# Kernel tuning notes

Measured on AMD Instinct MI355X. Metric: run time of the kernel, lower is better.

## Reference

```python
import jax, jax.numpy as jnp
import numpy as np

EPS = 1e-8

def setup_inputs() -> dict:
    key = jax.random.key(0)
    k1, k2, k3, k4, k5 = jax.random.split(key, 5)
    B, S, d, H = 4, 1024, 512, 8
    hd = d // H
    x = jax.random.normal(k1, (B, S, d), dtype=jnp.float32)
    V = jax.random.normal(k2, (B, S, H, hd), dtype=jnp.float32)
    # binary biological mask [B, S, S]
    M = (jax.random.uniform(k3, (B, S, S)) > 0.5).astype(jnp.float32)
    in_proj_w = jax.random.normal(k4, (3 * d, d), dtype=jnp.float32) * 0.02
    in_proj_b = jnp.zeros((3 * d,), dtype=jnp.float32)
    out_w = jax.random.normal(k5, (d, d), dtype=jnp.float32) * 0.02
    out_b = jnp.zeros((d,), dtype=jnp.float32)
    return {"x": x, "V": V, "M": M, "in_proj_w": in_proj_w,
            "in_proj_b": in_proj_b, "out_w": out_w, "out_b": out_b}


def reference(x, V, M, in_proj_w, in_proj_b, out_w, out_b):
    B, S, d = x.shape
    H, hd = V.shape[2], V.shape[3]
    # packed QKV projection (torch MHA in_proj); V slice is computed by torch
    # but its result is discarded, so only Q,K slices influence the output.
    qkv = x @ in_proj_w.T + in_proj_b            # [B, S, 3d]
    q = qkv[..., :d].reshape(B, S, H, hd).transpose(0, 2, 1, 3)        # [B,H,S,hd]
    k = qkv[..., d:2 * d].reshape(B, S, H, hd).transpose(0, 2, 1, 3)   # [B,H,S,hd]
    scores = jnp.einsum("bhqd,bhkd->bhqk", q, k) / jnp.sqrt(jnp.float32(hd))
    A = jax.nn.softmax(scores, axis=-1)           # [B,H,S,S] per-head attn weights
    # biological mask + L1 renormalization (post-hoc, as in original)
    A_sparse = A * M[:, None, :, :]
    norm = jnp.sum(jnp.abs(A_sparse), axis=-1, keepdims=True) + EPS
    A_bar = A_sparse / norm
    # custom V: [B,S,H,hd] -> [B,H,S,hd]
    Vp = V.transpose(0, 2, 1, 3)
    out = jnp.einsum("bhqk,bhkd->bhqd", A_bar, Vp)  # [B,H,S,hd]
    out = out.transpose(0, 2, 1, 3).reshape(B, S, d)
    return out @ out_w.T + out_b
```

## Files before the change

kernel.cpp:

```cpp
#include <hip/hip_runtime.h>
#include <hip/hip_bf16.h>

#define BB 4
#define SS 1024
#define DD 512
#define HH 8
#define HD 64

typedef __attribute__((ext_vector_type(8))) short bf16x8;
typedef __attribute__((ext_vector_type(4))) float f32x4;

static __device__ __forceinline__ unsigned short f2b(float f) {
  union { float f; unsigned int u; } c; c.f = f;
  return (unsigned short)((c.u + 0x7fffu + ((c.u >> 16) & 1u)) >> 16);
}

__global__ __launch_bounds__(256) void prep(
    const float* __restrict__ x, const float* __restrict__ W1,
    const float* __restrict__ Wo, const float* __restrict__ Mmask,
    const float* __restrict__ V, unsigned short* __restrict__ xb,
    unsigned short* __restrict__ W1b, unsigned short* __restrict__ Wob,
    unsigned char* __restrict__ Mpack, unsigned short* __restrict__ Vt) {
  __shared__ float Ls[64][65];
  const int bid = blockIdx.x;
  const int tid = threadIdx.x;

  if (bid < 1408) {
    const float* src; unsigned short* dst; size_t off;
    if (bid < 1024) { src = x;  dst = xb;  off = ((size_t)bid * 256 + tid) * 8; }
    else if (bid < 1280) { src = W1; dst = W1b; off = ((size_t)(bid - 1024) * 256 + tid) * 8; }
    else { src = Wo; dst = Wob; off = ((size_t)(bid - 1280) * 256 + tid) * 8; }
    const float4 a = *(const float4*)(src + off);
    const float4 b = *(const float4*)(src + off + 4);
    union { unsigned short s[8]; uint4 v; } o;
    o.s[0] = f2b(a.x); o.s[1] = f2b(a.y); o.s[2] = f2b(a.z); o.s[3] = f2b(a.w);
    o.s[4] = f2b(b.x); o.s[5] = f2b(b.y); o.s[6] = f2b(b.z); o.s[7] = f2b(b.w);
    *(uint4*)(dst + off) = o.v;
  } else if (bid < 3456) {
    const size_t g = (size_t)(bid - 1408) * 256 + tid;
    const float4 a = *(const float4*)(Mmask + g * 8);
    const float4 b = *(const float4*)(Mmask + g * 8 + 4);
    unsigned v = 0;
    v |= (a.x > 0.5f) ? 1u : 0u;   v |= (a.y > 0.5f) ? 2u : 0u;
    v |= (a.z > 0.5f) ? 4u : 0u;   v |= (a.w > 0.5f) ? 8u : 0u;
    v |= (b.x > 0.5f) ? 16u : 0u;  v |= (b.y > 0.5f) ? 32u : 0u;
    v |= (b.z > 0.5f) ? 64u : 0u;  v |= (b.w > 0.5f) ? 128u : 0u;
    Mpack[g] = (unsigned char)v;
  } else {
    const int id = bid - 3456;
    const int s0 = (id & 15) * 64, h = (id >> 4) & 7, b = id >> 7;
    {
      const int r = tid >> 2, cs = (tid & 3) * 16;
      const float* src = V + ((size_t)((b * SS + s0 + r) * HH) + h) * HD + cs;
#pragma unroll
      for (int j = 0; j < 4; j++) {
        const float4 v = *(const float4*)(src + j * 4);
        Ls[r][cs + j * 4 + 0] = v.x; Ls[r][cs + j * 4 + 1] = v.y;
        Ls[r][cs + j * 4 + 2] = v.z; Ls[r][cs + j * 4 + 3] = v.w;
      }
    }
    __syncthreads();
    {
      const int d = tid >> 2, ss = (tid & 3) * 16;
      union { unsigned short s[16]; uint4 v[2]; } o;
#pragma unroll
      for (int j = 0; j < 16; j++) o.s[j] = f2b(Ls[ss + j][d]);
      unsigned short* dst =
          Vt + ((size_t)((b * HH + h) * HD + d)) * SS + s0 + ss;
      *(uint4*)dst = o.v[0];
      *(uint4*)(dst + 8) = o.v[1];
    }
  }
}

__global__ __launch_bounds__(256) void gemm_qk(
    const unsigned short* __restrict__ xb, const unsigned short* __restrict__ W1b,
    const float* __restrict__ bias, unsigned short* __restrict__ qkb) {
  __shared__ unsigned short As[128][72];
  __shared__ unsigned short Bs[64][72];
  const int tid = threadIdx.x;
  const int lane = tid & 63, wave = tid >> 6;
  const int l16 = lane & 15, quad = lane >> 4;
  const int row0 = blockIdx.y * 128, col0 = blockIdx.x * 64;

  f32x4 acc[2][4];
#pragma unroll
  for (int i = 0; i < 2; i++)
#pragma unroll
    for (int j = 0; j < 4; j++) acc[i][j] = (f32x4){0.f, 0.f, 0.f, 0.f};

  for (int k0 = 0; k0 < DD; k0 += 64) {
    __syncthreads();
    {
      const int r = tid >> 1, cs = (tid & 1) * 32;
      const unsigned short* s = xb + (size_t)(row0 + r) * DD + k0 + cs;
#pragma unroll
      for (int j = 0; j < 4; j++)
        *(uint4*)&As[r][cs + j * 8] = *(const uint4*)(s + j * 8);
    }
    {
      const int r = tid >> 2, cs = (tid & 3) * 16;
      const unsigned short* s = W1b + (size_t)(col0 + r) * DD + k0 + cs;
      *(uint4*)&Bs[r][cs] = *(const uint4*)s;
      *(uint4*)&Bs[r][cs + 8] = *(const uint4*)(s + 8);
    }
    __syncthreads();

#pragma unroll
    for (int kk = 0; kk < 64; kk += 32) {
      const bf16x8 a0 = *(const bf16x8*)&As[wave * 32 + l16][kk + quad * 8];
      const bf16x8 a1 = *(const bf16x8*)&As[wave * 32 + 16 + l16][kk + quad * 8];
#pragma unroll
      for (int nt = 0; nt < 4; nt++) {
        const bf16x8 bb = *(const bf16x8*)&Bs[nt * 16 + l16][kk + quad * 8];
        acc[0][nt] = __builtin_amdgcn_mfma_f32_16x16x32_bf16(a0, bb, acc[0][nt], 0, 0, 0);
        acc[1][nt] = __builtin_amdgcn_mfma_f32_16x16x32_bf16(a1, bb, acc[1][nt], 0, 0, 0);
      }
    }
  }

#pragma unroll
  for (int nt = 0; nt < 4; nt++) {
    const int col = col0 + nt * 16 + l16;
    const float bv = bias[col];
    const float scale = (col < DD) ? 0.125f : 1.0f;
#pragma unroll
    for (int mi = 0; mi < 2; mi++)
#pragma unroll
      for (int reg = 0; reg < 4; reg++) {
        const int row = row0 + wave * 32 + mi * 16 + quad * 4 + reg;
        qkb[(size_t)row * 1024 + col] = f2b((acc[mi][nt][reg] + bv) * scale);
      }
  }
}

__global__ __launch_bounds__(256) void gemm_out(
    const unsigned short* __restrict__ Ab, const unsigned short* __restrict__ Wob,
    const float* __restrict__ bias, float* __restrict__ out) {
  __shared__ unsigned short As[128][72];
  __shared__ unsigned short Bs[64][72];
  const int tid = threadIdx.x;
  const int lane = tid & 63, wave = tid >> 6;
  const int l16 = lane & 15, quad = lane >> 4;
  const int row0 = blockIdx.y * 128, col0 = blockIdx.x * 64;

  f32x4 acc[2][4];
#pragma unroll
  for (int i = 0; i < 2; i++)
#pragma unroll
    for (int j = 0; j < 4; j++) acc[i][j] = (f32x4){0.f, 0.f, 0.f, 0.f};

  for (int k0 = 0; k0 < DD; k0 += 64) {
    __syncthreads();
    {
      const int r = tid >> 1, cs = (tid & 1) * 32;
      const unsigned short* s = Ab + (size_t)(row0 + r) * DD + k0 + cs;
#pragma unroll
      for (int j = 0; j < 4; j++)
        *(uint4*)&As[r][cs + j * 8] = *(const uint4*)(s + j * 8);
    }
    {
      const int r = tid >> 2, cs = (tid & 3) * 16;
      const unsigned short* s = Wob + (size_t)(col0 + r) * DD + k0 + cs;
      *(uint4*)&Bs[r][cs] = *(const uint4*)s;
      *(uint4*)&Bs[r][cs + 8] = *(const uint4*)(s + 8);
    }
    __syncthreads();

#pragma unroll
    for (int kk = 0; kk < 64; kk += 32) {
      const bf16x8 a0 = *(const bf16x8*)&As[wave * 32 + l16][kk + quad * 8];
      const bf16x8 a1 = *(const bf16x8*)&As[wave * 32 + 16 + l16][kk + quad * 8];
#pragma unroll
      for (int nt = 0; nt < 4; nt++) {
        const bf16x8 bb = *(const bf16x8*)&Bs[nt * 16 + l16][kk + quad * 8];
        acc[0][nt] = __builtin_amdgcn_mfma_f32_16x16x32_bf16(a0, bb, acc[0][nt], 0, 0, 0);
        acc[1][nt] = __builtin_amdgcn_mfma_f32_16x16x32_bf16(a1, bb, acc[1][nt], 0, 0, 0);
      }
    }
  }

#pragma unroll
  for (int nt = 0; nt < 4; nt++) {
    const int col = col0 + nt * 16 + l16;
    const float bv = bias[col];
#pragma unroll
    for (int mi = 0; mi < 2; mi++)
#pragma unroll
      for (int reg = 0; reg < 4; reg++) {
        const int row = row0 + wave * 32 + mi * 16 + quad * 4 + reg;
        out[(size_t)row * DD + col] = acc[mi][nt][reg] + bv;
      }
  }
}

__global__ __launch_bounds__(256) void flash_attn(
    const unsigned short* __restrict__ qkb, const unsigned short* __restrict__ Vt,
    const unsigned char* __restrict__ Mpack, unsigned short* __restrict__ attnb) {
  __shared__ unsigned short Qs[64][72];
  __shared__ unsigned short Ks[64][72];
  __shared__ unsigned short Vs[64][72];
  __shared__ unsigned short Ps[4][16][72];
  __shared__ float SmT[4][16];

  const int tid = threadIdx.x;
  const int lane = tid & 63, wave = tid >> 6;
  const int l16 = lane & 15, quad = lane >> 4;
  const int q0 = blockIdx.x * 64;
  const int h = blockIdx.y;
  const int b = blockIdx.z;

  {
    const int r = tid >> 2, cs = (tid & 3) * 16;
    const unsigned short* s = qkb + (size_t)(b * SS + q0 + r) * 1024 + h * HD + cs;
    *(uint4*)&Qs[r][cs] = *(const uint4*)s;
    *(uint4*)&Qs[r][cs + 8] = *(const uint4*)(s + 8);
  }
  const bf16x8 bQ0 = *(const bf16x8*)&Qs[wave * 16 + l16][quad * 8];
  const bf16x8 bQ1 = *(const bf16x8*)&Qs[wave * 16 + l16][32 + quad * 8];

  const unsigned char* mrowp =
      Mpack + (size_t)(b * SS + q0 + wave * 16 + l16) * 128;

  float Smp = 0.f;
  f32x4 O[4];
#pragma unroll
  for (int i = 0; i < 4; i++) O[i] = (f32x4){0.f, 0.f, 0.f, 0.f};

  const unsigned short* kbase = qkb + (size_t)(b * SS) * 1024 + DD + h * HD;
  const unsigned short* vbase = Vt + (size_t)((b * HH + h) * HD) * SS;

#pragma unroll 2
  for (int i = 0; i < 16; i++) {
    const uint2 mm = *(const uint2*)(mrowp + i * 8);

    __syncthreads();
    {
      const int r = tid >> 2, cs = (tid & 3) * 16;
      const unsigned short* s = kbase + (size_t)(i * 64 + r) * 1024 + cs;
      *(uint4*)&Ks[r][cs] = *(const uint4*)s;
      *(uint4*)&Ks[r][cs + 8] = *(const uint4*)(s + 8);
      const unsigned short* v = vbase + (size_t)r * SS + i * 64 + cs;
      *(uint4*)&Vs[r][cs] = *(const uint4*)v;
      *(uint4*)&Vs[r][cs + 8] = *(const uint4*)(v + 8);
    }
    __syncthreads();

#pragma unroll
    for (int t = 0; t < 4; t++) {
      const bf16x8 aK0 = *(const bf16x8*)&Ks[t * 16 + l16][quad * 8];
      const bf16x8 aK1 = *(const bf16x8*)&Ks[t * 16 + l16][32 + quad * 8];
      f32x4 a = (f32x4){0.f, 0.f, 0.f, 0.f};
      a = __builtin_amdgcn_mfma_f32_16x16x32_bf16(aK0, bQ0, a, 0, 0, 0);
      a = __builtin_amdgcn_mfma_f32_16x16x32_bf16(aK1, bQ1, a, 0, 0, 0);
      const unsigned nib =
          ((t < 2 ? mm.x : mm.y) >> ((t & 1) * 16 + quad * 4)) & 0xFu;
      float e0 = __expf(a[0]); e0 = (nib & 1u) ? e0 : 0.f;
      float e1 = __expf(a[1]); e1 = (nib & 2u) ? e1 : 0.f;
      float e2 = __expf(a[2]); e2 = (nib & 4u) ? e2 : 0.f;
      float e3 = __expf(a[3]); e3 = (nib & 8u) ? e3 : 0.f;
      Smp += (e0 + e1) + (e2 + e3);
      uint2 w;
      w.x = (unsigned)f2b(e0) | ((unsigned)f2b(e1) << 16);
      w.y = (unsigned)f2b(e2) | ((unsigned)f2b(e3) << 16);
      *(uint2*)&Ps[wave][l16][t * 16 + quad * 4] = w;
    }

    const bf16x8 aP0 = *(const bf16x8*)&Ps[wave][l16][quad * 8];
    const bf16x8 aP1 = *(const bf16x8*)&Ps[wave][l16][32 + quad * 8];
#pragma unroll
    for (int dt = 0; dt < 4; dt++) {
      const bf16x8 bV0 = *(const bf16x8*)&Vs[dt * 16 + l16][quad * 8];
      const bf16x8 bV1 = *(const bf16x8*)&Vs[dt * 16 + l16][32 + quad * 8];
      O[dt] = __builtin_amdgcn_mfma_f32_16x16x32_bf16(aP0, bV0, O[dt], 0, 0, 0);
      O[dt] = __builtin_amdgcn_mfma_f32_16x16x32_bf16(aP1, bV1, O[dt], 0, 0, 0);
    }
  }

  Smp += __shfl_xor(Smp, 16);
  Smp += __shfl_xor(Smp, 32);
  if (lane < 16) SmT[wave][lane] = Smp;
  float invr[4];
#pragma unroll
  for (int reg = 0; reg < 4; reg++)
    invr[reg] = 1.0f / (SmT[wave][quad * 4 + reg] + 1e-12f);
#pragma unroll
  for (int reg = 0; reg < 4; reg++) {
    const size_t row = (size_t)(b * SS + q0 + wave * 16 + quad * 4 + reg);
#pragma unroll
    for (int dt = 0; dt < 4; dt++)
      attnb[row * DD + h * HD + dt * 16 + l16] = f2b(O[dt][reg] * invr[reg]);
  }
}

extern "C" void kernel_launch(void* const* d_in, const int* in_sizes, int n_in,
                              void* d_out, int out_size, void* d_ws,
                              size_t ws_size, hipStream_t stream) {
  const float* x = (const float*)d_in[0];
  const float* V = (const float*)d_in[1];
  const float* Mmask = (const float*)d_in[2];
  const float* in_proj_w = (const float*)d_in[3];
  const float* in_proj_b = (const float*)d_in[4];
  const float* out_w = (const float*)d_in[5];
  const float* out_b = (const float*)d_in[6];
  float* out = (float*)d_out;

  unsigned char* ws = (unsigned char*)d_ws;
  unsigned short* qkb   = (unsigned short*)(ws);
  unsigned short* xb    = (unsigned short*)(ws + (8ull << 20));
  unsigned short* W1b   = (unsigned short*)(ws + (12ull << 20));
  unsigned short* Wob   = (unsigned short*)(ws + (13ull << 20));
  unsigned short* Vt    = (unsigned short*)(ws + (14ull << 20));
  unsigned short* attnb = (unsigned short*)(ws + (18ull << 20));
  unsigned char*  Mpack = ws + (22ull << 20);

  prep<<<3968, 256, 0, stream>>>(x, in_proj_w, out_w, Mmask, V,
                                 xb, W1b, Wob, Mpack, Vt);
  gemm_qk<<<dim3(16, 32), 256, 0, stream>>>(xb, W1b, in_proj_b, qkb);
  flash_attn<<<dim3(SS / 64, HH, BB), 256, 0, stream>>>(qkb, Vt, Mpack, attnb);
  gemm_out<<<dim3(8, 32), 256, 0, stream>>>(attnb, Wob, out_b, out);
}
```

Baseline: 149.6 us.

## Fuse all stages into one persistent kernel with grid-wide barriers

Merges the prep, QK projection, masked attention and output projection kernels into a single persistent kernel of 512 blocks. The stages are separated by atomic-counter grid barriers, and a union overlays their shared-memory buffers. The aim is to remove three kernel launch gaps and the tail drain between stages. The output GEMM is retiled to 64x64 so that it also fits exactly 512 blocks. In exchange, all blocks must be co-resident for the spin barriers to be safe, there is a memset launch per call, and the 64x64 tiles give less reuse in the final GEMM.

```diff
diff --git a/kernel.cpp b/kernel.cpp
--- a/kernel.cpp
+++ b/kernel.cpp
@@ -6,6 +6,7 @@
 #define DD 512
 #define HH 8
 #define HD 64
+#define NBLK 512u
 
 typedef __attribute__((ext_vector_type(8))) short bf16x8;
 typedef __attribute__((ext_vector_type(4))) float f32x4;
@@ -15,281 +16,275 @@
   return (unsigned short)((c.u + 0x7fffu + ((c.u >> 16) & 1u)) >> 16);
 }
 
-__global__ __launch_bounds__(256) void prep(
-    const float* __restrict__ x, const float* __restrict__ W1,
-    const float* __restrict__ Wo, const float* __restrict__ Mmask,
-    const float* __restrict__ V, unsigned short* __restrict__ xb,
-    unsigned short* __restrict__ W1b, unsigned short* __restrict__ Wob,
-    unsigned char* __restrict__ Mpack, unsigned short* __restrict__ Vt) {
-  __shared__ float Ls[64][65];
-  const int bid = blockIdx.x;
-  const int tid = threadIdx.x;
-
-  if (bid < 1408) {
-    const float* src; unsigned short* dst; size_t off;
-    if (bid < 1024) { src = x;  dst = xb;  off = ((size_t)bid * 256 + tid) * 8; }
-    else if (bid < 1280) { src = W1; dst = W1b; off = ((size_t)(bid - 1024) * 256 + tid) * 8; }
-    else { src = Wo; dst = Wob; off = ((size_t)(bid - 1280) * 256 + tid) * 8; }
-    const float4 a = *(const float4*)(src + off);
-    const float4 b = *(const float4*)(src + off + 4);
-    union { unsigned short s[8]; uint4 v; } o;
-    o.s[0] = f2b(a.x); o.s[1] = f2b(a.y); o.s[2] = f2b(a.z); o.s[3] = f2b(a.w);
-    o.s[4] = f2b(b.x); o.s[5] = f2b(b.y); o.s[6] = f2b(b.z); o.s[7] = f2b(b.w);
-    *(uint4*)(dst + off) = o.v;
-  } else if (bid < 3456) {
-    const size_t g = (size_t)(bid - 1408) * 256 + tid;
-    const float4 a = *(const float4*)(Mmask + g * 8);
-    const float4 b = *(const float4*)(Mmask + g * 8 + 4);
-    unsigned v = 0;
-    v |= (a.x > 0.5f) ? 1u : 0u;   v |= (a.y > 0.5f) ? 2u : 0u;
-    v |= (a.z > 0.5f) ? 4u : 0u;   v |= (a.w > 0.5f) ? 8u : 0u;
-    v |= (b.x > 0.5f) ? 16u : 0u;  v |= (b.y > 0.5f) ? 32u : 0u;
-    v |= (b.z > 0.5f) ? 64u : 0u;  v |= (b.w > 0.5f) ? 128u : 0u;
-    Mpack[g] = (unsigned char)v;
-  } else {
-    const int id = bid - 3456;
-    const int s0 = (id & 15) * 64, h = (id >> 4) & 7, b = id >> 7;
-    {
-      const int r = tid >> 2, cs = (tid & 3) * 16;
-      const float* src = V + ((size_t)((b * SS + s0 + r) * HH) + h) * HD + cs;
-#pragma unroll
-      for (int j = 0; j < 4; j++) {
-        const float4 v = *(const float4*)(src + j * 4);
-        Ls[r][cs + j * 4 + 0] = v.x; Ls[r][cs + j * 4 + 1] = v.y;
-        Ls[r][cs + j * 4 + 2] = v.z; Ls[r][cs + j * 4 + 3] = v.w;
-      }
-    }
-    __syncthreads();
-    {
-      const int d = tid >> 2, ss = (tid & 3) * 16;
-      union { unsigned short s[16]; uint4 v[2]; } o;
-#pragma unroll
-      for (int j = 0; j < 16; j++) o.s[j] = f2b(Ls[ss + j][d]);
-      unsigned short* dst =
-          Vt + ((size_t)((b * HH + h) * HD + d)) * SS + s0 + ss;
-      *(uint4*)dst = o.v[0];
-      *(uint4*)(dst + 8) = o.v[1];
-    }
-  }
+static __device__ __forceinline__ void grid_barrier(unsigned* cnt) {
+  __threadfence();
+  __syncthreads();
+  if (threadIdx.x == 0) {
+    __hip_atomic_fetch_add(cnt, 1u, __ATOMIC_ACQ_REL, __HIP_MEMORY_SCOPE_AGENT);
+    while (__hip_atomic_load(cnt, __ATOMIC_ACQUIRE, __HIP_MEMORY_SCOPE_AGENT) <
+           NBLK)
+      __builtin_amdgcn_s_sleep(2);
+  }
+  __syncthreads();
+  __threadfence();
 }
 
-__global__ __launch_bounds__(256) void gemm_qk(
-    const unsigned short* __restrict__ xb, const unsigned short* __restrict__ W1b,
-    const float* __restrict__ bias, unsigned short* __restrict__ qkb) {
-  __shared__ unsigned short As[128][72];
-  __shared__ unsigned short Bs[64][72];
+union SharedU {
+  struct { float Ls[64][65]; } pr;
+  struct { unsigned short As[128][72], Bs[64][72]; } gm;
+  struct {
+    unsigned short Qs[64][72], Ks[64][72], Vs[64][72], Ps[4][16][72];
+    float SmT[4][16];
+  } fl;
+};
+
+__global__ __launch_bounds__(256, 2) void fused(
+    const float* __restrict__ x, const float* __restrict__ V,
+    const float* __restrict__ Mmask, const float* __restrict__ W1,
+    const float* __restrict__ b1, const float* __restrict__ Wo,
+    const float* __restrict__ bo, float* __restrict__ out,
+    unsigned short* __restrict__ xb, unsigned short* __restrict__ W1b,
+    unsigned short* __restrict__ Wob, unsigned short* __restrict__ qkb,
+    unsigned short* __restrict__ Vt, unsigned short* __restrict__ attnb,
+    unsigned char* __restrict__ Mpack, unsigned* __restrict__ cnts) {
+  __shared__ SharedU sh;
   const int tid = threadIdx.x;
   const int lane = tid & 63, wave = tid >> 6;
   const int l16 = lane & 15, quad = lane >> 4;
-  const int row0 = blockIdx.y * 128, col0 = blockIdx.x * 64;
-
-  f32x4 acc[2][4];
-#pragma unroll
-  for (int i = 0; i < 2; i++)
-#pragma unroll
-    for (int j = 0; j < 4; j++) acc[i][j] = (f32x4){0.f, 0.f, 0.f, 0.f};
-
-  for (int k0 = 0; k0 < DD; k0 += 64) {
-    __syncthreads();
-    {
-      const int r = tid >> 1, cs = (tid & 1) * 32;
-      const unsigned short* s = xb + (size_t)(row0 + r) * DD + k0 + cs;
-#pragma unroll
-      for (int j = 0; j < 4; j++)
-        *(uint4*)&As[r][cs + j * 8] = *(const uint4*)(s + j * 8);
-    }
+
+  for (int u = blockIdx.x; u < 3968; u += NBLK) {
+    if (u < 1408) {
+      const float* src; unsigned short* dst; size_t off;
+      if (u < 1024) { src = x;  dst = xb;  off = ((size_t)u * 256 + tid) * 8; }
+      else if (u < 1280) { src = W1; dst = W1b; off = ((size_t)(u - 1024) * 256 + tid) * 8; }
+      else { src = Wo; dst = Wob; off = ((size_t)(u - 1280) * 256 + tid) * 8; }
+      const float4 a = *(const float4*)(src + off);
+      const float4 b = *(const float4*)(src + off + 4);
+      union { unsigned short s[8]; uint4 v; } o;
+      o.s[0] = f2b(a.x); o.s[1] = f2b(a.y); o.s[2] = f2b(a.z); o.s[3] = f2b(a.w);
+      o.s[4] = f2b(b.x); o.s[5] = f2b(b.y); o.s[6] = f2b(b.z); o.s[7] = f2b(b.w);
+      *(uint4*)(dst + off) = o.v;
+    } else if (u < 3456) {
+      const size_t g = (size_t)(u - 1408) * 256 + tid;
+      const float4 a = *(const float4*)(Mmask + g * 8);
+      const float4 b = *(const float4*)(Mmask + g * 8 + 4);
+      unsigned v = 0;
+      v |= (a.x > 0.5f) ? 1u : 0u;   v |= (a.y > 0.5f) ? 2u : 0u;
+      v |= (a.z > 0.5f) ? 4u : 0u;   v |= (a.w > 0.5f) ? 8u : 0u;
+      v |= (b.x > 0.5f) ? 16u : 0u;  v |= (b.y > 0.5f) ? 32u : 0u;
+      v |= (b.z > 0.5f) ? 64u : 0u;  v |= (b.w > 0.5f) ? 128u : 0u;
+      Mpack[g] = (unsigned char)v;
+    } else {
+      const int id = u - 3456;
+      const int s0 = (id & 15) * 64, h = (id >> 4) & 7, b = id >> 7;
+      {
+        const int r = tid >> 2, cs = (tid & 3) * 16;
+        const float* src = V + ((size_t)((b * SS + s0 + r) * HH) + h) * HD + cs;
+#pragma unroll
+        for (int j = 0; j < 4; j++) {
+          const float4 v = *(const float4*)(src + j * 4);
+          sh.pr.Ls[r][cs + j * 4 + 0] = v.x; sh.pr.Ls[r][cs + j * 4 + 1] = v.y;
+          sh.pr.Ls[r][cs + j * 4 + 2] = v.z; sh.pr.Ls[r][cs + j * 4 + 3] = v.w;
+        }
+      }
+      __syncthreads();
+      {
+        const int d = tid >> 2, ss = (tid & 3) * 16;
+        union { unsigned short s[16]; uint4 v[2]; } o;
+#pragma unroll
+        for (int j = 0; j < 16; j++) o.s[j] = f2b(sh.pr.Ls[ss + j][d]);
+        unsigned short* dst =
+            Vt + ((size_t)((b * HH + h) * HD + d)) * SS + s0 + ss;
+        *(uint4*)dst = o.v[0];
+        *(uint4*)(dst + 8) = o.v[1];
+      }
+      __syncthreads();
+    }
+  }
+  grid_barrier(&cnts[0]);
+
+  {
+    const int u = blockIdx.x;
+    const int row0 = (u >> 4) * 128, col0 = (u & 15) * 64;
+    f32x4 acc[2][4];
+#pragma unroll
+    for (int i = 0; i < 2; i++)
+#pragma unroll
+      for (int j = 0; j < 4; j++) acc[i][j] = (f32x4){0.f, 0.f, 0.f, 0.f};
+
+    for (int k0 = 0; k0 < DD; k0 += 64) {
+      __syncthreads();
+      {
+        const int r = tid >> 1, cs = (tid & 1) * 32;
+        const unsigned short* s = xb + (size_t)(row0 + r) * DD + k0 + cs;
+#pragma unroll
+        for (int j = 0; j < 4; j++)
+          *(uint4*)&sh.gm.As[r][cs + j * 8] = *(const uint4*)(s + j * 8);
+      }
+      {
+        const int r = tid >> 2, cs = (tid & 3) * 16;
+        const unsigned short* s = W1b + (size_t)(col0 + r) * DD + k0 + cs;
+        *(uint4*)&sh.gm.Bs[r][cs] = *(const uint4*)s;
+        *(uint4*)&sh.gm.Bs[r][cs + 8] = *(const uint4*)(s + 8);
+      }
+      __syncthreads();
+#pragma unroll
+      for (int kk = 0; kk < 64; kk += 32) {
+        const bf16x8 a0 = *(const bf16x8*)&sh.gm.As[wave * 32 + l16][kk + quad * 8];
+        const bf16x8 a1 = *(const bf16x8*)&sh.gm.As[wave * 32 + 16 + l16][kk + quad * 8];
+#pragma unroll
+        for (int nt = 0; nt < 4; nt++) {
+          const bf16x8 bb = *(const bf16x8*)&sh.gm.Bs[nt * 16 + l16][kk + quad * 8];
+          acc[0][nt] = __builtin_amdgcn_mfma_f32_16x16x32_bf16(a0, bb, acc[0][nt], 0, 0, 0);
+          acc[1][nt] = __builtin_amdgcn_mfma_f32_16x16x32_bf16(a1, bb, acc[1][nt], 0, 0, 0);
+        }
+      }
+    }
+#pragma unroll
+    for (int nt = 0; nt < 4; nt++) {
+      const int col = col0 + nt * 16 + l16;
+      const float bv = b1[col];
+      const float scale = (col < DD) ? 0.125f : 1.0f;
+#pragma unroll
+      for (int mi = 0; mi < 2; mi++)
+#pragma unroll
+        for (int reg = 0; reg < 4; reg++) {
+          const int row = row0 + wave * 32 + mi * 16 + quad * 4 + reg;
+          qkb[(size_t)row * 1024 + col] = f2b((acc[mi][nt][reg] + bv) * scale);
+        }
+    }
+  }
+  grid_barrier(&cnts[1]);
+
+  {
+    const int u = blockIdx.x;
+    const int q0 = (u & 15) * 64;
+    const int h = (u >> 4) & 7;
+    const int b = u >> 7;
+
     {
       const int r = tid >> 2, cs = (tid & 3) * 16;
-      const unsigned short* s = W1b + (size_t)(col0 + r) * DD + k0 + cs;
-      *(uint4*)&Bs[r][cs] = *(const uint4*)s;
-      *(uint4*)&Bs[r][cs + 8] = *(const uint4*)(s + 8);
-    }
-    __syncthreads();
-
-#pragma unroll
-    for (int kk = 0; kk < 64; kk += 32) {
-      const bf16x8 a0 = *(const bf16x8*)&As[wave * 32 + l16][kk + quad * 8];
-      const bf16x8 a1 = *(const bf16x8*)&As[wave * 32 + 16 + l16][kk + quad * 8];
-#pragma unroll
-      for (int nt = 0; nt < 4; nt++) {
-        const bf16x8 bb = *(const bf16x8*)&Bs[nt * 16 + l16][kk + quad * 8];
-        acc[0][nt] = __builtin_amdgcn_mfma_f32_16x16x32_bf16(a0, bb, acc[0][nt], 0, 0, 0);
-        acc[1][nt] = __builtin_amdgcn_mfma_f32_16x16x32_bf16(a1, bb, acc[1][nt], 0, 0, 0);
-      }
-    }
-  }
-
-#pragma unroll
-  for (int nt = 0; nt < 4; nt++) {
-    const int col = col0 + nt * 16 + l16;
-    const float bv = bias[col];
-    const float scale = (col < DD) ? 0.125f : 1.0f;
-#pragma unroll
-    for (int mi = 0; mi < 2; mi++)
+      const unsigned short* s =
+          qkb + (size_t)(b * SS + q0 + r) * 1024 + h * HD + cs;
+      *(uint4*)&sh.fl.Qs[r][cs] = *(const uint4*)s;
+      *(uint4*)&sh.fl.Qs[r][cs + 8] = *(const uint4*)(s + 8);
+    }
+    const bf16x8 bQ0 = *(const bf16x8*)&sh.fl.Qs[wave * 16 + l16][quad * 8];
+    const bf16x8 bQ1 = *(const bf16x8*)&sh.fl.Qs[wave * 16 + l16][32 + quad * 8];
+
+    const unsigned char* mrowp =
+        Mpack + (size_t)(b * SS + q0 + wave * 16 + l16) * 128;
+
+    float Smp = 0.f;
+    f32x4 O[4];
+#pragma unroll
+    for (int i = 0; i < 4; i++) O[i] = (f32x4){0.f, 0.f, 0.f, 0.f};
+
+    const unsigned short* kbase = qkb + (size_t)(b * SS) * 1024 + DD + h * HD;
+    const unsigned short* vbase = Vt + (size_t)((b * HH + h) * HD) * SS;
+
+#pragma unroll 2
+    for (int i = 0; i < 16; i++) {
+      const uint2 mm = *(const uint2*)(mrowp + i * 8);
+      __syncthreads();
+      {
+        const int r = tid >> 2, cs = (tid & 3) * 16;
+        const unsigned short* s = kbase + (size_t)(i * 64 + r) * 1024 + cs;
+        *(uint4*)&sh.fl.Ks[r][cs] = *(const uint4*)s;
+        *(uint4*)&sh.fl.Ks[r][cs + 8] = *(const uint4*)(s + 8);
+        const unsigned short* v = vbase + (size_t)r * SS + i * 64 + cs;
+        *(uint4*)&sh.fl.Vs[r][cs] = *(const uint4*)v;
+        *(uint4*)&sh.fl.Vs[r][cs + 8] = *(const uint4*)(v + 8);
+      }
+      __syncthreads();
+
+#pragma unroll
+      for (int t = 0; t < 4; t++) {
+        const bf16x8 aK0 = *(const bf16x8*)&sh.fl.Ks[t * 16 + l16][quad * 8];
+        const bf16x8 aK1 = *(const bf16x8*)&sh.fl.Ks[t * 16 + l16][32 + quad * 8];
+        f32x4 a = (f32x4){0.f, 0.f, 0.f, 0.f};
+        a = __builtin_amdgcn_mfma_f32_16x16x32_bf16(aK0, bQ0, a, 0, 0, 0);
+        a = __builtin_amdgcn_mfma_f32_16x16x32_bf16(aK1, bQ1, a, 0, 0, 0);
+        const unsigned nib =
+            ((t < 2 ? mm.x : mm.y) >> ((t & 1) * 16 + quad * 4)) & 0xFu;
+        float e0 = __expf(a[0]); e0 = (nib & 1u) ? e0 : 0.f;
+        float e1 = __expf(a[1]); e1 = (nib & 2u) ? e1 : 0.f;
+        float e2 = __expf(a[2]); e2 = (nib & 4u) ? e2 : 0.f;
+        float e3 = __expf(a[3]); e3 = (nib & 8u) ? e3 : 0.f;
+        Smp += (e0 + e1) + (e2 + e3);
+        uint2 w;
+        w.x = (unsigned)f2b(e0) | ((unsigned)f2b(e1) << 16);
+        w.y = (unsigned)f2b(e2) | ((unsigned)f2b(e3) << 16);
+        *(uint2*)&sh.fl.Ps[wave][l16][t * 16 + quad * 4] = w;
+      }
+
+      const bf16x8 aP0 = *(const bf16x8*)&sh.fl.Ps[wave][l16][quad * 8];
+      const bf16x8 aP1 = *(const bf16x8*)&sh.fl.Ps[wave][l16][32 + quad * 8];
+#pragma unroll
+      for (int dt = 0; dt < 4; dt++) {
+        const bf16x8 bV0 = *(const bf16x8*)&sh.fl.Vs[dt * 16 + l16][quad * 8];
+        const bf16x8 bV1 = *(const bf16x8*)&sh.fl.Vs[dt * 16 + l16][32 + quad * 8];
+        O[dt] = __builtin_amdgcn_mfma_f32_16x16x32_bf16(aP0, bV0, O[dt], 0, 0, 0);
+        O[dt] = __builtin_amdgcn_mfma_f32_16x16x32_bf16(aP1, bV1, O[dt], 0, 0, 0);
+      }
+    }
+
+    Smp += __shfl_xor(Smp, 16);
+    Smp += __shfl_xor(Smp, 32);
+    if (lane < 16) sh.fl.SmT[wave][lane] = Smp;
+    float invr[4];
+#pragma unroll
+    for (int reg = 0; reg < 4; reg++)
+      invr[reg] = 1.0f / (sh.fl.SmT[wave][quad * 4 + reg] + 1e-12f);
+#pragma unroll
+    for (int reg = 0; reg < 4; reg++) {
+      const size_t row = (size_t)(b * SS + q0 + wave * 16 + quad * 4 + reg);
+#pragma unroll
+      for (int dt = 0; dt < 4; dt++)
+        attnb[row * DD + h * HD + dt * 16 + l16] = f2b(O[dt][reg] * invr[reg]);
+    }
+  }
+  grid_barrier(&cnts[2]);
+
+  {
+    const int u = blockIdx.x;
+    const int row0 = (u >> 3) * 64, col0 = (u & 7) * 64;
+    f32x4 acc[4];
+#pragma unroll
+    for (int j = 0; j < 4; j++) acc[j] = (f32x4){0.f, 0.f, 0.f, 0.f};
+
+    for (int k0 = 0; k0 < DD; k0 += 64) {
+      __syncthreads();
+      {
+        const int r = tid >> 2, cs = (tid & 3) * 16;
+        const unsigned short* s = attnb + (size_t)(row0 + r) * DD + k0 + cs;
+        *(uint4*)&sh.gm.As[r][cs] = *(const uint4*)s;
+        *(uint4*)&sh.gm.As[r][cs + 8] = *(const uint4*)(s + 8);
+        const unsigned short* w = Wob + (size_t)(col0 + r) * DD + k0 + cs;
+        *(uint4*)&sh.gm.Bs[r][cs] = *(const uint4*)w;
+        *(uint4*)&sh.gm.Bs[r][cs + 8] = *(const uint4*)(w + 8);
+      }
+      __syncthreads();
+#pragma unroll
+      for (int kk = 0; kk < 64; kk += 32) {
+        const bf16x8 a0 = *(const bf16x8*)&sh.gm.As[wave * 16 + l16][kk + quad * 8];
+#pragma unroll
+        for (int nt = 0; nt < 4; nt++) {
+          const bf16x8 bb = *(const bf16x8*)&sh.gm.Bs[nt * 16 + l16][kk + quad * 8];
+          acc[nt] = __builtin_amdgcn_mfma_f32_16x16x32_bf16(a0, bb, acc[nt], 0, 0, 0);
+        }
+      }
+    }
+#pragma unroll
+    for (int nt = 0; nt < 4; nt++) {
+      const int col = col0 + nt * 16 + l16;
+      const float bv = bo[col];
 #pragma unroll
       for (int reg = 0; reg < 4; reg++) {
-        const int row = row0 + wave * 32 + mi * 16 + quad * 4 + reg;
-        qkb[(size_t)row * 1024 + col] = f2b((acc[mi][nt][reg] + bv) * scale);
-      }
-  }
-}
-
-__global__ __launch_bounds__(256) void gemm_out(
-    const unsigned short* __restrict__ Ab, const unsigned short* __restrict__ Wob,
-    const float* __restrict__ bias, float* __restrict__ out) {
-  __shared__ unsigned short As[128][72];
-  __shared__ unsigned short Bs[64][72];
-  const int tid = threadIdx.x;
-  const int lane = tid & 63, wave = tid >> 6;
-  const int l16 = lane & 15, quad = lane >> 4;
-  const int row0 = blockIdx.y * 128, col0 = blockIdx.x * 64;
-
-  f32x4 acc[2][4];
-#pragma unroll
-  for (int i = 0; i < 2; i++)
-#pragma unroll
-    for (int j = 0; j < 4; j++) acc[i][j] = (f32x4){0.f, 0.f, 0.f, 0.f};
-
-  for (int k0 = 0; k0 < DD; k0 += 64) {
-    __syncthreads();
-    {
-      const int r = tid >> 1, cs = (tid & 1) * 32;
-      const unsigned short* s = Ab + (size_t)(row0 + r) * DD + k0 + cs;
-#pragma unroll
-      for (int j = 0; j < 4; j++)
-        *(uint4*)&As[r][cs + j * 8] = *(const uint4*)(s + j * 8);
-    }
-    {
-      const int r = tid >> 2, cs = (tid & 3) * 16;
-      const unsigned short* s = Wob + (size_t)(col0 + r) * DD + k0 + cs;
-      *(uint4*)&Bs[r][cs] = *(const uint4*)s;
-      *(uint4*)&Bs[r][cs + 8] = *(const uint4*)(s + 8);
-    }
-    __syncthreads();
-
-#pragma unroll
-    for (int kk = 0; kk < 64; kk += 32) {
-      const bf16x8 a0 = *(const bf16x8*)&As[wave * 32 + l16][kk + quad * 8];
-      const bf16x8 a1 = *(const bf16x8*)&As[wave * 32 + 16 + l16][kk + quad * 8];
-#pragma unroll
-      for (int nt = 0; nt < 4; nt++) {
-        const bf16x8 bb = *(const bf16x8*)&Bs[nt * 16 + l16][kk + quad * 8];
-        acc[0][nt] = __builtin_amdgcn_mfma_f32_16x16x32_bf16(a0, bb, acc[0][nt], 0, 0, 0);
-        acc[1][nt] = __builtin_amdgcn_mfma_f32_16x16x32_bf16(a1, bb, acc[1][nt], 0, 0, 0);
-      }
-    }
-  }
-
-#pragma unroll
-  for (int nt = 0; nt < 4; nt++) {
-    const int col = col0 + nt * 16 + l16;
-    const float bv = bias[col];
-#pragma unroll
-    for (int mi = 0; mi < 2; mi++)
-#pragma unroll
-      for (int reg = 0; reg < 4; reg++) {
-        const int row = row0 + wave * 32 + mi * 16 + quad * 4 + reg;
-        out[(size_t)row * DD + col] = acc[mi][nt][reg] + bv;
-      }
-  }
-}
-
-__global__ __launch_bounds__(256) void flash_attn(
-    const unsigned short* __restrict__ qkb, const unsigned short* __restrict__ Vt,
-    const unsigned char* __restrict__ Mpack, unsigned short* __restrict__ attnb) {
-  __shared__ unsigned short Qs[64][72];
-  __shared__ unsigned short Ks[64][72];
-  __shared__ unsigned short Vs[64][72];
-  __shared__ unsigned short Ps[4][16][72];
-  __shared__ float SmT[4][16];
-
-  const int tid = threadIdx.x;
-  const int lane = tid & 63, wave = tid >> 6;
-  const int l16 = lane & 15, quad = lane >> 4;
-  const int q0 = blockIdx.x * 64;
-  const int h = blockIdx.y;
-  const int b = blockIdx.z;
-
-  {
-    const int r = tid >> 2, cs = (tid & 3) * 16;
-    const unsigned short* s = qkb + (size_t)(b * SS + q0 + r) * 1024 + h * HD + cs;
-    *(uint4*)&Qs[r][cs] = *(const uint4*)s;
-    *(uint4*)&Qs[r][cs + 8] = *(const uint4*)(s + 8);
-  }
-  const bf16x8 bQ0 = *(const bf16x8*)&Qs[wave * 16 + l16][quad * 8];
-  const bf16x8 bQ1 = *(const bf16x8*)&Qs[wave * 16 + l16][32 + quad * 8];
-
-  const unsigned char* mrowp =
-      Mpack + (size_t)(b * SS + q0 + wave * 16 + l16) * 128;
-
-  float Smp = 0.f;
-  f32x4 O[4];
-#pragma unroll
-  for (int i = 0; i < 4; i++) O[i] = (f32x4){0.f, 0.f, 0.f, 0.f};
-
-  const unsigned short* kbase = qkb + (size_t)(b * SS) * 1024 + DD + h * HD;
-  const unsigned short* vbase = Vt + (size_t)((b * HH + h) * HD) * SS;
-
-#pragma unroll 2
-  for (int i = 0; i < 16; i++) {
-    const uint2 mm = *(const uint2*)(mrowp + i * 8);
-
-    __syncthreads();
-    {
-      const int r = tid >> 2, cs = (tid & 3) * 16;
-      const unsigned short* s = kbase + (size_t)(i * 64 + r) * 1024 + cs;
-      *(uint4*)&Ks[r][cs] = *(const uint4*)s;
-      *(uint4*)&Ks[r][cs + 8] = *(const uint4*)(s + 8);
-      const unsigned short* v = vbase + (size_t)r * SS + i * 64 + cs;
-      *(uint4*)&Vs[r][cs] = *(const uint4*)v;
-      *(uint4*)&Vs[r][cs + 8] = *(const uint4*)(v + 8);
-    }
-    __syncthreads();
-
-#pragma unroll
-    for (int t = 0; t < 4; t++) {
-      const bf16x8 aK0 = *(const bf16x8*)&Ks[t * 16 + l16][quad * 8];
-      const bf16x8 aK1 = *(const bf16x8*)&Ks[t * 16 + l16][32 + quad * 8];
-      f32x4 a = (f32x4){0.f, 0.f, 0.f, 0.f};
-      a = __builtin_amdgcn_mfma_f32_16x16x32_bf16(aK0, bQ0, a, 0, 0, 0);
-      a = __builtin_amdgcn_mfma_f32_16x16x32_bf16(aK1, bQ1, a, 0, 0, 0);
-      const unsigned nib =
-          ((t < 2 ? mm.x : mm.y) >> ((t & 1) * 16 + quad * 4)) & 0xFu;
-      float e0 = __expf(a[0]); e0 = (nib & 1u) ? e0 : 0.f;
-      float e1 = __expf(a[1]); e1 = (nib & 2u) ? e1 : 0.f;
-      float e2 = __expf(a[2]); e2 = (nib & 4u) ? e2 : 0.f;
-      float e3 = __expf(a[3]); e3 = (nib & 8u) ? e3 : 0.f;
-      Smp += (e0 + e1) + (e2 + e3);
-      uint2 w;
-      w.x = (unsigned)f2b(e0) | ((unsigned)f2b(e1) << 16);
-      w.y = (unsigned)f2b(e2) | ((unsigned)f2b(e3) << 16);
-      *(uint2*)&Ps[wave][l16][t * 16 + quad * 4] = w;
-    }
-
-    const bf16x8 aP0 = *(const bf16x8*)&Ps[wave][l16][quad * 8];
-    const bf16x8 aP1 = *(const bf16x8*)&Ps[wave][l16][32 + quad * 8];
-#pragma unroll
-    for (int dt = 0; dt < 4; dt++) {
-      const bf16x8 bV0 = *(const bf16x8*)&Vs[dt * 16 + l16][quad * 8];
-      const bf16x8 bV1 = *(const bf16x8*)&Vs[dt * 16 + l16][32 + quad * 8];
-      O[dt] = __builtin_amdgcn_mfma_f32_16x16x32_bf16(aP0, bV0, O[dt], 0, 0, 0);
-      O[dt] = __builtin_amdgcn_mfma_f32_16x16x32_bf16(aP1, bV1, O[dt], 0, 0, 0);
-    }
-  }
-
-  Smp += __shfl_xor(Smp, 16);
-  Smp += __shfl_xor(Smp, 32);
-  if (lane < 16) SmT[wave][lane] = Smp;
-  float invr[4];
-#pragma unroll
-  for (int reg = 0; reg < 4; reg++)
-    invr[reg] = 1.0f / (SmT[wave][quad * 4 + reg] + 1e-12f);
-#pragma unroll
-  for (int reg = 0; reg < 4; reg++) {
-    const size_t row = (size_t)(b * SS + q0 + wave * 16 + quad * 4 + reg);
-#pragma unroll
-    for (int dt = 0; dt < 4; dt++)
-      attnb[row * DD + h * HD + dt * 16 + l16] = f2b(O[dt][reg] * invr[reg]);
+        const int row = row0 + wave * 16 + quad * 4 + reg;
+        out[(size_t)row * DD + col] = acc[nt][reg] + bv;
+      }
+    }
   }
 }
 
@@ -313,10 +308,10 @@
   unsigned short* Vt    = (unsigned short*)(ws + (14ull << 20));
   unsigned short* attnb = (unsigned short*)(ws + (18ull << 20));
   unsigned char*  Mpack = ws + (22ull << 20);
-
-  prep<<<3968, 256, 0, stream>>>(x, in_proj_w, out_w, Mmask, V,
-                                 xb, W1b, Wob, Mpack, Vt);
-  gemm_qk<<<dim3(16, 32), 256, 0, stream>>>(xb, W1b, in_proj_b, qkb);
-  flash_attn<<<dim3(SS / 64, HH, BB), 256, 0, stream>>>(qkb, Vt, Mpack, attnb);
-  gemm_out<<<dim3(8, 32), 256, 0, stream>>>(attnb, Wob, out_b, out);
+  unsigned*       cnts  = (unsigned*)(ws + (23ull << 20));
+
+  hipMemsetAsync(cnts, 0, 64, stream);
+  fused<<<NBLK, 256, 0, stream>>>(x, V, Mmask, in_proj_w, in_proj_b, out_w,
+                                  out_b, out, xb, W1b, Wob, qkb, Vt, attnb,
+                                  Mpack, cnts);
 }
```

New measurement: 534.1 us. 3.57x slower.
